# Kernel tuning notes

Measured on AMD Instinct MI355X. Metric: run time of the kernel, lower is better.

## Reference

```python
import jax, jax.numpy as jnp
import numpy as np

B, S, F, H = 4, 1024, 512, 16
D = F // H  # head_dim = 32

def setup_inputs() -> dict:
    key = jax.random.key(0)
    ks = jax.random.split(key, 9)
    init = lambda k, shp: 0.1 * jax.random.normal(k, shp, dtype=jnp.float32)
    return {
        "kv": jax.random.normal(ks[0], (B, S, F), dtype=jnp.float32),
        "q": jax.random.normal(ks[1], (B, S, F), dtype=jnp.float32),
        "mask": jnp.ones((B, 1, S, S), dtype=jnp.int32),
        "Wq": init(ks[2], (F, F)),
        "Wk": init(ks[3], (F, F)),
        "Wv": init(ks[4], (F, F)),
        "Wo": init(ks[5], (F, F)),
        "rel_table": init(ks[6], (2 * S + 1, D)),  # nn.Embed(2*length_q+1, head_dim)
        "Wrel": init(ks[7], (D, D)),  # rel_pos_dense, no bias
    }

def reference(kv, q, mask, Wq, Wk, Wv, Wo, rel_table, Wrel):
    b, s, f = q.shape
    h, d = H, f // H
    qh = (q @ Wq).reshape(b, s, h, d)
    kh = (kv @ Wk).reshape(b, s, h, d)
    vh = (kv @ Wv).reshape(b, s, h, d)
    # raw content scores [b,h,q,k]
    scores = jnp.einsum('bqhd,bkhd->bhqk', qh, kh)
    # relative-position embedding: dist in [0, 2s], table lookup + dense
    dist = jnp.arange(s)[None, :] - jnp.arange(s)[:, None] + s  # [q,k]
    emb = rel_table[dist] @ Wrel  # [q,k,d]
    scores = scores + jnp.einsum('bqhd,qkd->bhqk', qh, emb)
    scores = scores / jnp.sqrt(jnp.asarray(d, scores.dtype))
    # mask-select before softmax (mask [b,1,q,k] broadcast over heads)
    scores = jnp.where(mask > 0, scores, -jnp.inf)
    attn = jax.nn.softmax(scores, axis=-1)
    out = jnp.einsum('bhqk,bkhd->bqhd', attn, vh).reshape(b, s, f)
    return out @ Wo  # dropout is identity (training=False)
```

## Files before the change

kernel.cpp:

```cpp
#include <hip/hip_runtime.h>

#define S_ 1024
#define H_ 16
#define D_ 32

typedef float f32x4 __attribute__((ext_vector_type(4)));
typedef short bf16x8 __attribute__((ext_vector_type(8)));
typedef unsigned long long u64;

static __device__ __forceinline__ short f2b(float f) {
    union { float f; unsigned u; } x; x.f = f;
    unsigned u = x.u;
    unsigned r = u + 0x7fffu + ((u >> 16) & 1u);
    return (short)(r >> 16);
}
static __device__ __forceinline__ unsigned pk_rne(float lo, float hi) {
    union { float f; unsigned u; } a, b; a.f = lo; b.f = hi;
    unsigned ul = a.u + 0x7fffu + ((a.u >> 16) & 1u);
    unsigned uh = b.u + 0x7fffu + ((b.u >> 16) & 1u);
    return __builtin_amdgcn_perm(uh, ul, 0x07060302u);
}
static __device__ __forceinline__ unsigned pk_trunc(float lo, float hi) {
    union { float f; unsigned u; } a, b; a.f = lo; b.f = hi;
    return __builtin_amdgcn_perm(b.u, a.u, 0x07060302u);
}
static __device__ __forceinline__ float bperm(int bidx, float v) {
    union { float f; int i; } x; x.f = v;
    x.i = __builtin_amdgcn_ds_bpermute(bidx, x.i);
    return x.f;
}
static __device__ __forceinline__ int stg64(int row, int c8) {
    return row * 72 + (c8 ^ ((row & 3) << 3));
}

__global__ __launch_bounds__(256)
void prep_kernel(const float* __restrict__ rt, short* __restrict__ relb,
                 const int* __restrict__ mask, u64* __restrict__ mbits,
                 const float* __restrict__ Wq, const float* __restrict__ Wk,
                 const float* __restrict__ Wv, const float* __restrict__ Wo,
                 short* __restrict__ Wt)
{
    __shared__ float ls[32][33];
    int bid = blockIdx.x, t = threadIdx.x;
    if (bid < 257) {
        int i = bid * 256 + t;
        if (i < 2049 * 32) relb[i] = f2b(rt[i]);
        return;
    }
    bid -= 257;
    if (bid < 4096) {
        #pragma unroll
        for (int j = 0; j < 4; ++j) {
            int i = bid * 1024 + j * 256 + t;
            u64 bal = __ballot(mask[i] > 0);
            if ((t & 63) == 0) mbits[i >> 6] = bal;
        }
        return;
    }
    bid -= 4096;
    int mat = bid >> 8, tl = bid & 255, ti = tl >> 4, tj = tl & 15;
    const float* W = (mat == 0) ? Wq : (mat == 1) ? Wk : (mat == 2) ? Wv : Wo;
    int r = t >> 3, c = (t & 7) * 4;
    float4 v = *(const float4*)(W + (long)(ti * 32 + r) * 512 + tj * 32 + c);
    ls[r][c] = v.x; ls[r][c + 1] = v.y; ls[r][c + 2] = v.z; ls[r][c + 3] = v.w;
    __syncthreads();
    int nl = t >> 3, kk = (t & 7) * 4;
    uint2 o = { pk_rne(ls[kk][nl], ls[kk + 1][nl]),
                pk_rne(ls[kk + 2][nl], ls[kk + 3][nl]) };
    *(uint2*)(Wt + ((long)mat * 512 + tj * 32 + nl) * 512 + ti * 32 + kk) = o;
}

__global__ __launch_bounds__(256)
void gemm3_kernel(const float* __restrict__ q, const float* __restrict__ kv,
                  const short* __restrict__ Wt,
                  short* __restrict__ qh, short* __restrict__ kh, short* __restrict__ vt,
                  float scale)
{
    __shared__ __align__(16) short a_s[64 * 72];
    __shared__ __align__(16) short b_s[64 * 72];
    const int t = threadIdx.x;
    const int w = t >> 6, lane = t & 63, l15 = lane & 15, quad = lane >> 4;
    const int wm = w & 1, wn = w >> 1;

    int bid = blockIdx.x;
    const int mat = bid >> 9;
    const int rr_ = bid & 511;
    const int bm = (rr_ >> 3) * 64, bn = (rr_ & 7) * 64;
    const float* A = (mat == 0) ? q : kv;
    const short* Wm = Wt + (long)mat * 262144;

    const int srow = t >> 2, scg = (t & 3) << 4;
    f32x4 acc[2][2] = {};

    for (int k0 = 0; k0 < 512; k0 += 64) {
        {
            const float* ap = A + (long)(bm + srow) * 512 + k0 + scg;
            float4 v0 = *(const float4*)(ap);
            float4 v1 = *(const float4*)(ap + 4);
            float4 v2 = *(const float4*)(ap + 8);
            float4 v3 = *(const float4*)(ap + 12);
            uint4 o0 = { pk_rne(v0.x, v0.y), pk_rne(v0.z, v0.w),
                         pk_rne(v1.x, v1.y), pk_rne(v1.z, v1.w) };
            uint4 o1 = { pk_rne(v2.x, v2.y), pk_rne(v2.z, v2.w),
                         pk_rne(v3.x, v3.y), pk_rne(v3.z, v3.w) };
            *(uint4*)(a_s + stg64(srow, scg)) = o0;
            *(uint4*)(a_s + stg64(srow, scg + 8)) = o1;
        }
        {
            const short* bp = Wm + (long)(bn + srow) * 512 + k0 + scg;
            *(bf16x8*)(b_s + stg64(srow, scg))     = *(const bf16x8*)(bp);
            *(bf16x8*)(b_s + stg64(srow, scg + 8)) = *(const bf16x8*)(bp + 8);
        }
        __syncthreads();
        bf16x8 af[2][2], bfr[2][2];
        #pragma unroll
        for (int i = 0; i < 2; ++i)
            #pragma unroll
            for (int ks = 0; ks < 2; ++ks) {
                af[i][ks]  = *(const bf16x8*)(a_s + stg64(wm * 32 + i * 16 + l15, ks * 32 + quad * 8));
                bfr[i][ks] = *(const bf16x8*)(b_s + stg64(wn * 32 + i * 16 + l15, ks * 32 + quad * 8));
            }
        if (mat == 2) {
            #pragma unroll
            for (int i = 0; i < 2; ++i)
                #pragma unroll
                for (int j = 0; j < 2; ++j)
                    #pragma unroll
                    for (int ks = 0; ks < 2; ++ks)
                        acc[i][j] = __builtin_amdgcn_mfma_f32_16x16x32_bf16(bfr[i][ks], af[j][ks], acc[i][j], 0, 0, 0);
        } else {
            #pragma unroll
            for (int i = 0; i < 2; ++i)
                #pragma unroll
                for (int j = 0; j < 2; ++j)
                    #pragma unroll
                    for (int ks = 0; ks < 2; ++ks)
                        acc[i][j] = __builtin_amdgcn_mfma_f32_16x16x32_bf16(af[i][ks], bfr[j][ks], acc[i][j], 0, 0, 0);
        }
        __syncthreads();
    }

    if (mat < 2) {
        short* out = (mat == 0) ? qh : kh;
        float alpha = (mat == 0) ? scale : 1.0f;
        #pragma unroll
        for (int i = 0; i < 2; ++i)
            #pragma unroll
            for (int j = 0; j < 2; ++j)
                #pragma unroll
                for (int r = 0; r < 4; ++r) {
                    int m = bm + wm * 32 + i * 16 + quad * 4 + r;
                    int n = bn + wn * 32 + j * 16 + l15;
                    int bb = m >> 10, s = m & 1023, hh = n >> 5, dd = n & 31;
                    out[((long)((bb * 16 + hh) * 1024 + s)) * 32 + dd] = f2b(acc[i][j][r] * alpha);
                }
    } else {
        #pragma unroll
        for (int i = 0; i < 2; ++i)
            #pragma unroll
            for (int j = 0; j < 2; ++j)
                #pragma unroll
                for (int r = 0; r < 4; ++r) {
                    int n = bn + wn * 32 + i * 16 + quad * 4 + r;
                    int m = bm + wm * 32 + j * 16 + l15;
                    int bb = m >> 10, s = m & 1023, hh = n >> 5, dd = n & 31;
                    int sp = (s & ~63) | ((s & 15) << 2) | ((s >> 4) & 3);
                    vt[((long)((bb * 16 + hh) * 32 + dd)) * 1024 + sp] = f2b(acc[i][j][r]);
                }
    }
}

__global__ __launch_bounds__(256)
void gemm_out_kernel(const short* __restrict__ ao, const short* __restrict__ Wt,
                     float* __restrict__ out)
{
    __shared__ __align__(16) short a_s[64 * 72];
    __shared__ __align__(16) short b_s[64 * 72];
    const int t = threadIdx.x;
    const int w = t >> 6, lane = t & 63, l15 = lane & 15, quad = lane >> 4;
    const int wm = w & 1, wn = w >> 1;
    const int bm = (blockIdx.x >> 3) * 64, bn = (blockIdx.x & 7) * 64;
    const short* Wm = Wt + (long)3 * 262144;
    const int srow = t >> 2, scg = (t & 3) << 4;
    f32x4 acc[2][2] = {};

    for (int k0 = 0; k0 < 512; k0 += 64) {
        {
            const short* apb = ao + (long)(bm + srow) * 512 + k0 + scg;
            *(bf16x8*)(a_s + stg64(srow, scg))     = *(const bf16x8*)(apb);
            *(bf16x8*)(a_s + stg64(srow, scg + 8)) = *(const bf16x8*)(apb + 8);
            const short* bpb = Wm + (long)(bn + srow) * 512 + k0 + scg;
            *(bf16x8*)(b_s + stg64(srow, scg))     = *(const bf16x8*)(bpb);
            *(bf16x8*)(b_s + stg64(srow, scg + 8)) = *(const bf16x8*)(bpb + 8);
        }
        __syncthreads();
        bf16x8 af[2][2], bfr[2][2];
        #pragma unroll
        for (int i = 0; i < 2; ++i)
            #pragma unroll
            for (int ks = 0; ks < 2; ++ks) {
                af[i][ks]  = *(const bf16x8*)(a_s + stg64(wm * 32 + i * 16 + l15, ks * 32 + quad * 8));
                bfr[i][ks] = *(const bf16x8*)(b_s + stg64(wn * 32 + i * 16 + l15, ks * 32 + quad * 8));
            }
        #pragma unroll
        for (int i = 0; i < 2; ++i)
            #pragma unroll
            for (int j = 0; j < 2; ++j)
                #pragma unroll
                for (int ks = 0; ks < 2; ++ks)
                    acc[i][j] = __builtin_amdgcn_mfma_f32_16x16x32_bf16(af[i][ks], bfr[j][ks], acc[i][j], 0, 0, 0);
        __syncthreads();
    }
    #pragma unroll
    for (int i = 0; i < 2; ++i)
        #pragma unroll
        for (int j = 0; j < 2; ++j)
            #pragma unroll
            for (int r = 0; r < 4; ++r) {
                int m = bm + wm * 32 + i * 16 + quad * 4 + r;
                int n = bn + wn * 32 + j * 16 + l15;
                out[(long)m * 512 + n] = acc[i][j][r];
            }
}

__global__ __launch_bounds__(256, 4)
void attn_kernel(const short* __restrict__ qh, const float* __restrict__ wrel,
                 const short* __restrict__ kh, const short* __restrict__ vt,
                 const short* __restrict__ relb, const u64* __restrict__ mbits,
                 short* __restrict__ ao)
{
    __shared__ __align__(16) short smem[4 * 2 * 16 * 72];
    const int t = threadIdx.x;
    const int w = t >> 6, lane = t & 63, l15 = lane & 15, quad = lane >> 4;
    short* pw0 = smem + w * (2 * 16 * 72);
    short* pw1 = pw0 + 16 * 72;

    const int half = w & 1, qsel = w >> 1;
    const int gw = blockIdx.x * 2 + qsel;
    const int qt = gw & 63, h = (gw >> 6) & 15, b = gw >> 10;
    const int q0 = qt * 16, bh = b * H_ + h;
    const int c0 = half * 8;

    const long qbase = ((long)bh * S_ + q0 + l15) * D_ + quad * 8;
    const bf16x8 a_qh = *(const bf16x8*)(qh + qbase);
    const long kv_bh = (long)bh * S_ * D_;
    const u64* mrow = mbits + ((long)b * S_ + q0 + quad * 4) * 16;

    bf16x8 a_qr;
    {
        #pragma unroll
        for (int nt = 0; nt < 2; ++nt) {
            const float* wp = wrel + (long)(nt * 16 + l15) * 32 + quad * 8;
            float4 w0 = *(const float4*)(wp);
            float4 w1 = *(const float4*)(wp + 4);
            bf16x8 bw;
            *(uint4*)&bw = (uint4){ pk_rne(w0.x, w0.y), pk_rne(w0.z, w0.w),
                                    pk_rne(w1.x, w1.y), pk_rne(w1.z, w1.w) };
            f32x4 z = {0.f, 0.f, 0.f, 0.f};
            f32x4 cq = __builtin_amdgcn_mfma_f32_16x16x32_bf16(a_qh, bw, z, 0, 0, 0);
            #pragma unroll
            for (int r = 0; r < 4; ++r)
                pw0[(quad * 4 + r) * 36 + nt * 16 + l15] = f2b(cq[r]);
        }
        asm volatile("" ::: "memory");
        a_qr = *(const bf16x8*)(pw0 + l15 * 36 + quad * 8);
        asm volatile("" ::: "memory");
    }

    int bidx[4]; int cnd[4];
    #pragma unroll
    for (int r = 0; r < 4; ++r) {
        int qq = quad * 4 + r;
        bidx[r] = (quad * 16 + ((l15 + 15 - qq) & 15)) * 4;
        cnd[r] = (l15 > qq);
    }

    f32x4 oacc[2] = {};
    float l4[4] = {0.f, 0.f, 0.f, 0.f};

    bf16x8 preg0 = {}, preg1 = {};
    bf16x8 bv00 = {}, bv01 = {}, bv10 = {}, bv11 = {};

    bf16x8 kf[4], rf[5];
    {
        const int ub0 = c0 * 64 - q0 + (S_ - 15);
        #pragma unroll
        for (int ut = 0; ut < 5; ++ut)
            rf[ut] = *(const bf16x8*)(relb + (long)(ub0 + ut * 16 + l15) * D_ + quad * 8);
        #pragma unroll
        for (int kt = 0; kt < 4; ++kt)
            kf[kt] = *(const bf16x8*)(kh + kv_bh + (long)(c0 * 64 + kt * 16 + l15) * D_ + quad * 8);
    }

    for (int i = 0; i < 8; ++i) {
        const int c = c0 + i;
        const int kbase = c * 64;
        short* pwbuf = (i & 1) ? pw1 : pw0;

        f32x4 ctf[5], sc[4];
        #pragma unroll
        for (int ut = 0; ut < 5; ++ut) {
            f32x4 z = {0.f, 0.f, 0.f, 0.f};
            ctf[ut] = __builtin_amdgcn_mfma_f32_16x16x32_bf16(a_qr, rf[ut], z, 0, 0, 0);
        }
        #pragma unroll
        for (int kt = 0; kt < 4; ++kt) {
            f32x4 z = {0.f, 0.f, 0.f, 0.f};
            sc[kt] = __builtin_amdgcn_mfma_f32_16x16x32_bf16(a_qh, kf[kt], z, 0, 0, 0);
        }
        if (i) {
            oacc[0] = __builtin_amdgcn_mfma_f32_16x16x32_bf16(preg0, bv00, oacc[0], 0, 0, 0);
            oacc[1] = __builtin_amdgcn_mfma_f32_16x16x32_bf16(preg0, bv01, oacc[1], 0, 0, 0);
            oacc[0] = __builtin_amdgcn_mfma_f32_16x16x32_bf16(preg1, bv10, oacc[0], 0, 0, 0);
            oacc[1] = __builtin_amdgcn_mfma_f32_16x16x32_bf16(preg1, bv11, oacc[1], 0, 0, 0);
        }
        {
            const int cn = c + ((i < 7) ? 1 : 0);
            const int kbn = cn * 64, ubn = kbn - q0 + (S_ - 15);
            #pragma unroll
            for (int ut = 0; ut < 5; ++ut)
                rf[ut] = *(const bf16x8*)(relb + (long)(ubn + ut * 16 + l15) * D_ + quad * 8);
            #pragma unroll
            for (int kt = 0; kt < 4; ++kt)
                kf[kt] = *(const bf16x8*)(kh + kv_bh + (long)(kbn + kt * 16 + l15) * D_ + quad * 8);
        }
        bv00 = *(const bf16x8*)(vt + kv_bh + (long)(l15) * S_ + kbase + quad * 8);
        bv01 = *(const bf16x8*)(vt + kv_bh + (long)(16 + l15) * S_ + kbase + quad * 8);
        bv10 = *(const bf16x8*)(vt + kv_bh + (long)(l15) * S_ + kbase + 32 + quad * 8);
        bv11 = *(const bf16x8*)(vt + kv_bh + (long)(16 + l15) * S_ + kbase + 32 + quad * 8);

        #pragma unroll
        for (int r = 0; r < 4; ++r) {
            float tt[5];
            #pragma unroll
            for (int ut = 0; ut < 5; ++ut) tt[ut] = bperm(bidx[r], ctf[ut][r]);
            float s0 = sc[0][r] + (cnd[r] ? tt[1] : tt[0]);
            float s1 = sc[1][r] + (cnd[r] ? tt[2] : tt[1]);
            float s2 = sc[2][r] + (cnd[r] ? tt[3] : tt[2]);
            float s3 = sc[3][r] + (cnd[r] ? tt[4] : tt[3]);
            u64 mw = mrow[r * 16 + c] >> l15;
            unsigned lo = (unsigned)mw, hi = (unsigned)(mw >> 32);
            float p0 = __expf(s0); p0 = (lo & 1u)         ? p0 : 0.f;
            float p1 = __expf(s1); p1 = ((lo >> 16) & 1u) ? p1 : 0.f;
            float p2 = __expf(s2); p2 = (hi & 1u)         ? p2 : 0.f;
            float p3 = __expf(s3); p3 = ((hi >> 16) & 1u) ? p3 : 0.f;
            l4[r] += (p0 + p1) + (p2 + p3);
            u64 pv = ((u64)pk_trunc(p2, p3) << 32) | (u64)pk_trunc(p0, p1);
            *(u64*)(pwbuf + (quad * 4 + r) * 72 + l15 * 4) = pv;
        }
        asm volatile("" ::: "memory");
        preg0 = *(const bf16x8*)(pwbuf + l15 * 72 + quad * 8);
        preg1 = *(const bf16x8*)(pwbuf + l15 * 72 + 32 + quad * 8);
    }
    oacc[0] = __builtin_amdgcn_mfma_f32_16x16x32_bf16(preg0, bv00, oacc[0], 0, 0, 0);
    oacc[1] = __builtin_amdgcn_mfma_f32_16x16x32_bf16(preg0, bv01, oacc[1], 0, 0, 0);
    oacc[0] = __builtin_amdgcn_mfma_f32_16x16x32_bf16(preg1, bv10, oacc[0], 0, 0, 0);
    oacc[1] = __builtin_amdgcn_mfma_f32_16x16x32_bf16(preg1, bv11, oacc[1], 0, 0, 0);

    #pragma unroll
    for (int r = 0; r < 4; ++r) {
        float l = l4[r];
        l += __shfl_xor(l, 1, 64);
        l += __shfl_xor(l, 2, 64);
        l += __shfl_xor(l, 4, 64);
        l += __shfl_xor(l, 8, 64);
        l4[r] = l;
    }

    asm volatile("" ::: "memory");
    float* fo = (float*)pw0;
    float* fl = (float*)pw1;
    #pragma unroll
    for (int r = 0; r < 4; ++r) {
        #pragma unroll
        for (int dt = 0; dt < 2; ++dt)
            fo[(quad * 4 + r) * 32 + dt * 16 + l15] = oacc[dt][r];
        if (l15 == 0) fl[quad * 4 + r] = l4[r];
    }
    __syncthreads();
    if (half == 0) {
        const float* po = (const float*)(smem + (w ^ 1) * (2 * 16 * 72));
        const float* pl = po + 576;
        #pragma unroll
        for (int r = 0; r < 4; ++r) {
            int row = quad * 4 + r;
            float inv = 1.0f / (l4[r] + pl[row]);
            #pragma unroll
            for (int dt = 0; dt < 2; ++dt) {
                float o = oacc[dt][r] + po[row * 32 + dt * 16 + l15];
                ao[((long)(b * S_ + q0 + row) * H_ + h) * D_ + dt * 16 + l15] = f2b(o * inv);
            }
        }
    }
}

extern "C" void kernel_launch(void* const* d_in, const int* in_sizes, int n_in,
                              void* d_out, int out_size, void* d_ws, size_t ws_size,
                              hipStream_t stream) {
    (void)in_sizes; (void)n_in; (void)out_size; (void)ws_size;
    const float* kv   = (const float*)d_in[0];
    const float* q    = (const float*)d_in[1];
    const int*   mask = (const int*)d_in[2];
    const float* Wq   = (const float*)d_in[3];
    const float* Wk   = (const float*)d_in[4];
    const float* Wv   = (const float*)d_in[5];
    const float* Wo   = (const float*)d_in[6];
    const float* rt   = (const float*)d_in[7];
    const float* Wrel = (const float*)d_in[8];

    char* ws = (char*)d_ws;
    short* qh   = (short*)(ws);
    short* kh   = (short*)(ws + (4u  << 20));
    short* vt   = (short*)(ws + (8u  << 20));
    short* ao   = (short*)(ws + (12u << 20));
    short* Wt   = (short*)(ws + (16u << 20));
    short* relb = (short*)(ws + (18u << 20));
    u64*  mbits = (u64*) (ws + (18u << 20) + (256u << 10));

    const float scale = 0.17677669529663687f;

    prep_kernel<<<257 + 4096 + 1024, 256, 0, stream>>>(
        rt, relb, mask, mbits, Wq, Wk, Wv, Wo, Wt);

    gemm3_kernel<<<1536, 256, 0, stream>>>(q, kv, Wt, qh, kh, vt, scale);

    attn_kernel<<<2048, 256, 0, stream>>>(qh, Wrel, kh, vt, relb, mbits, ao);

    gemm_out_kernel<<<512, 256, 0, stream>>>(ao, Wt, (float*)d_out);
}
```

Measured before the change: 227.7 us.

## Drop K/rel register prefetch in attention, reorder GEMM tile grid

Result: faster. 191.9 us (-15.7%).

```diff
diff --git a/kernel.cpp b/kernel.cpp
--- a/kernel.cpp
+++ b/kernel.cpp
@@ -85,7 +85,7 @@
     int bid = blockIdx.x;
     const int mat = bid >> 9;
     const int rr_ = bid & 511;
-    const int bm = (rr_ >> 3) * 64, bn = (rr_ & 7) * 64;
+    const int bm = (rr_ & 63) * 64, bn = (rr_ >> 6) * 64;
     const float* A = (mat == 0) ? q : kv;
     const short* Wm = Wt + (long)mat * 262144;
 
@@ -179,7 +179,7 @@
     const int t = threadIdx.x;
     const int w = t >> 6, lane = t & 63, l15 = lane & 15, quad = lane >> 4;
     const int wm = w & 1, wn = w >> 1;
-    const int bm = (blockIdx.x >> 3) * 64, bn = (blockIdx.x & 7) * 64;
+    const int bm = (blockIdx.x & 63) * 64, bn = (blockIdx.x >> 6) * 64;
     const short* Wm = Wt + (long)3 * 262144;
     const int srow = t >> 2, scg = (t & 3) << 4;
     f32x4 acc[2][2] = {};
@@ -223,7 +223,7 @@
             }
 }
 
-__global__ __launch_bounds__(256, 4)
+__global__ __launch_bounds__(256)
 void attn_kernel(const short* __restrict__ qh, const float* __restrict__ wrel,
                  const short* __restrict__ kh, const short* __restrict__ vt,
                  const short* __restrict__ relb, const u64* __restrict__ mbits,
@@ -267,46 +267,50 @@
         asm volatile("" ::: "memory");
     }
 
-    int bidx[4]; int cnd[4];
+    int bidx[4];
     #pragma unroll
-    for (int r = 0; r < 4; ++r) {
-        int qq = quad * 4 + r;
-        bidx[r] = (quad * 16 + ((l15 + 15 - qq) & 15)) * 4;
-        cnd[r] = (l15 > qq);
-    }
+    for (int r = 0; r < 4; ++r)
+        bidx[r] = (quad * 16 + ((l15 + 15 - (quad * 4 + r)) & 15)) * 4;
 
     f32x4 oacc[2] = {};
     float l4[4] = {0.f, 0.f, 0.f, 0.f};
 
     bf16x8 preg0 = {}, preg1 = {};
     bf16x8 bv00 = {}, bv01 = {}, bv10 = {}, bv11 = {};
-
-    bf16x8 kf[4], rf[5];
-    {
-        const int ub0 = c0 * 64 - q0 + (S_ - 15);
-        #pragma unroll
-        for (int ut = 0; ut < 5; ++ut)
-            rf[ut] = *(const bf16x8*)(relb + (long)(ub0 + ut * 16 + l15) * D_ + quad * 8);
-        #pragma unroll
-        for (int kt = 0; kt < 4; ++kt)
-            kf[kt] = *(const bf16x8*)(kh + kv_bh + (long)(c0 * 64 + kt * 16 + l15) * D_ + quad * 8);
-    }
 
     for (int i = 0; i < 8; ++i) {
         const int c = c0 + i;
         const int kbase = c * 64;
+        const int ub = kbase - q0 + (S_ - 15);
         short* pwbuf = (i & 1) ? pw1 : pw0;
 
-        f32x4 ctf[5], sc[4];
-        #pragma unroll
-        for (int ut = 0; ut < 5; ++ut) {
+        float bb[4][4];
+        {
+            f32x4 ctf[5];
+            #pragma unroll
+            for (int ut = 0; ut < 5; ++ut) {
+                bf16x8 bre = *(const bf16x8*)(relb + (long)(ub + ut * 16 + l15) * D_ + quad * 8);
+                f32x4 z = {0.f, 0.f, 0.f, 0.f};
+                ctf[ut] = __builtin_amdgcn_mfma_f32_16x16x32_bf16(a_qr, bre, z, 0, 0, 0);
+            }
+            #pragma unroll
+            for (int r = 0; r < 4; ++r) {
+                int cnd = l15 > quad * 4 + r;
+                float tt[5];
+                #pragma unroll
+                for (int ut = 0; ut < 5; ++ut) tt[ut] = bperm(bidx[r], ctf[ut][r]);
+                bb[r][0] = cnd ? tt[1] : tt[0];
+                bb[r][1] = cnd ? tt[2] : tt[1];
+                bb[r][2] = cnd ? tt[3] : tt[2];
+                bb[r][3] = cnd ? tt[4] : tt[3];
+            }
+        }
+        f32x4 sc[4];
+        #pragma unroll
+        for (int kt = 0; kt < 4; ++kt) {
+            bf16x8 bk = *(const bf16x8*)(kh + kv_bh + (long)(kbase + kt * 16 + l15) * D_ + quad * 8);
             f32x4 z = {0.f, 0.f, 0.f, 0.f};
-            ctf[ut] = __builtin_amdgcn_mfma_f32_16x16x32_bf16(a_qr, rf[ut], z, 0, 0, 0);
-        }
-        #pragma unroll
-        for (int kt = 0; kt < 4; ++kt) {
-            f32x4 z = {0.f, 0.f, 0.f, 0.f};
-            sc[kt] = __builtin_amdgcn_mfma_f32_16x16x32_bf16(a_qh, kf[kt], z, 0, 0, 0);
+            sc[kt] = __builtin_amdgcn_mfma_f32_16x16x32_bf16(a_qh, bk, z, 0, 0, 0);
         }
         if (i) {
             oacc[0] = __builtin_amdgcn_mfma_f32_16x16x32_bf16(preg0, bv00, oacc[0], 0, 0, 0);
@@ -314,16 +318,6 @@
             oacc[0] = __builtin_amdgcn_mfma_f32_16x16x32_bf16(preg1, bv10, oacc[0], 0, 0, 0);
             oacc[1] = __builtin_amdgcn_mfma_f32_16x16x32_bf16(preg1, bv11, oacc[1], 0, 0, 0);
         }
-        {
-            const int cn = c + ((i < 7) ? 1 : 0);
-            const int kbn = cn * 64, ubn = kbn - q0 + (S_ - 15);
-            #pragma unroll
-            for (int ut = 0; ut < 5; ++ut)
-                rf[ut] = *(const bf16x8*)(relb + (long)(ubn + ut * 16 + l15) * D_ + quad * 8);
-            #pragma unroll
-            for (int kt = 0; kt < 4; ++kt)
-                kf[kt] = *(const bf16x8*)(kh + kv_bh + (long)(kbn + kt * 16 + l15) * D_ + quad * 8);
-        }
         bv00 = *(const bf16x8*)(vt + kv_bh + (long)(l15) * S_ + kbase + quad * 8);
         bv01 = *(const bf16x8*)(vt + kv_bh + (long)(16 + l15) * S_ + kbase + quad * 8);
         bv10 = *(const bf16x8*)(vt + kv_bh + (long)(l15) * S_ + kbase + 32 + quad * 8);
@@ -331,13 +325,10 @@
 
         #pragma unroll
         for (int r = 0; r < 4; ++r) {
-            float tt[5];
-            #pragma unroll
-            for (int ut = 0; ut < 5; ++ut) tt[ut] = bperm(bidx[r], ctf[ut][r]);
-            float s0 = sc[0][r] + (cnd[r] ? tt[1] : tt[0]);
-            float s1 = sc[1][r] + (cnd[r] ? tt[2] : tt[1]);
-            float s2 = sc[2][r] + (cnd[r] ? tt[3] : tt[2]);
-            float s3 = sc[3][r] + (cnd[r] ? tt[4] : tt[3]);
+            float s0 = sc[0][r] + bb[r][0];
+            float s1 = sc[1][r] + bb[r][1];
+            float s2 = sc[2][r] + bb[r][2];
+            float s3 = sc[3][r] + bb[r][3];
             u64 mw = mrow[r * 16 + c] >> l15;
             unsigned lo = (unsigned)mw, hi = (unsigned)(mw >> 32);
             float p0 = __expf(s0); p0 = (lo & 1u)         ? p0 : 0.f;
```
